# Optimization experiments

Hardware: AMD Instinct MI355X
Metric: run time of the kernel (lower is better)

The kernel has to match this reference:

```python
import jax, jax.numpy as jnp
import numpy as np

B, C, F_IN, F_OUT = 4096, 63, 250, 250
NEG_SLOPE = 0.2  # GATConv default negative_slope


def setup_inputs() -> dict:
    key = jax.random.key(0)
    ks = jax.random.split(key, 5)
    return {
        "x": jax.random.normal(ks[0], (B, 1, C, F_IN), dtype=jnp.float32),
        "W": jax.random.normal(ks[1], (F_IN, F_OUT), dtype=jnp.float32) / np.sqrt(F_IN),
        "att_src": jax.random.normal(ks[2], (F_OUT,), dtype=jnp.float32) / np.sqrt(F_OUT),
        "att_dst": jax.random.normal(ks[3], (F_OUT,), dtype=jnp.float32) / np.sqrt(F_OUT),
        "bias": jax.random.normal(ks[4], (F_OUT,), dtype=jnp.float32) * 0.01,
    }


def reference(x, W, att_src, att_dst, bias):
    # x: [B, 1, C, F_in] -> per-batch graph of C=63 nodes, fully connected
    # (all i!=j edges plus GATConv's default self-loops => dense C x C attention).
    h = jnp.einsum("bcf,fo->bco", x[:, 0], W)          # [B, C, F_out] node embeddings
    a_s = jnp.einsum("bco,o->bc", h, att_src)           # per-source score
    a_d = jnp.einsum("bco,o->bc", h, att_dst)           # per-destination score
    # e[b, dst, src] = leakyrelu(a_s[src] + a_d[dst]); softmax over sources per dst
    e = jax.nn.leaky_relu(a_s[:, None, :] + a_d[:, :, None], NEG_SLOPE)  # [B, C, C]
    alpha = jax.nn.softmax(e, axis=-1)
    out = jnp.einsum("bds,bso->bdo", alpha, h) + bias   # [B, C, F_out]
    return out[:, None]                                  # [B, 1, C, F_out]
```

## Files before the change

### kernel.cpp

```cpp
#include <hip/hip_runtime.h>
#include <hip/hip_bf16.h>

typedef __bf16 bf16;
typedef __attribute__((ext_vector_type(8))) __bf16 bf16x8;
typedef __attribute__((ext_vector_type(4))) __bf16 bf16x4;
typedef __attribute__((ext_vector_type(2))) __bf16 bf16x2;
typedef __attribute__((ext_vector_type(4))) float f32x4;

#define C_NODES 63
#define F_DIM   250
#define NEG_SLOPE 0.2f

#define OFF_AS    32000
#define OFF_AD    32256
#define LDS_BYTES 32768

__device__ __forceinline__ int swz(int a) { return a ^ ((a >> 3) & 0x70); }
__device__ __forceinline__ int swzA(int a) {
    return a ^ ((((a >> 8) & 3) ^ ((a >> 10) & 3)) << 4) ^ (((a >> 12) & 1) << 6);
}

extern "C" __global__ __launch_bounds__(256)
void gat_prep(const float* __restrict__ W, const float* __restrict__ att_src,
              const float* __restrict__ att_dst, bf16* __restrict__ Wp) {
    int i = blockIdx.x * 256 + threadIdx.x;
    int tile = i >> 9;
    int ln   = (i >> 3) & 63;
    int j    = i & 7;
    int kt = tile >> 4, nt = tile & 15;
    int k = kt * 32 + (ln >> 4) * 8 + j;
    int n = nt * 16 + (ln & 15);
    float v = 0.f;
    if (k < F_DIM) {
        if (n < F_DIM) {
            v = W[k * F_DIM + n];
        } else if (n == F_DIM || n == F_DIM + 1) {
            const float* att = (n == F_DIM) ? att_src : att_dst;
            float s = 0.f;
            for (int o = 0; o < F_DIM; ++o) s = fmaf(W[k * F_DIM + o], att[o], s);
            v = s;
        }
    }
    Wp[i] = (bf16)v;
}

extern "C" __global__ __launch_bounds__(256, 4)
void gat_main(const float* __restrict__ x, const bf16* __restrict__ Wp,
              const float* __restrict__ bias, float* __restrict__ out)
{
    __shared__ __align__(16) unsigned char smem[LDS_BYTES];
    const int tid  = threadIdx.x;
    const int lane = tid & 63;
    const int w    = tid >> 6;
    const int b    = blockIdx.x;
    const int fl   = lane & 15;
    const int fh   = lane >> 4;

    const bf16x8* wpv = (const bf16x8*)Wp;

    if (tid < 64) {
        int base = swzA((((tid >> 4) * 8 + 7) << 10) + (48 + (tid & 15)) * 16);
        *(unsigned int*)(smem + base + 4) = 0u;
        *(unsigned long long*)(smem + base + 8) = 0ull;
    } else if (tid < 96) {
        int idx = tid - 64;
        int base = swzA(((24 + (idx >> 2)) << 10) + ((((idx & 3) << 4) | 15) * 16));
        *(f32x4*)(smem + base) = (f32x4){0.f, 0.f, 0.f, 0.f};
    }

    {
        const float* xb = x + (size_t)b * (C_NODES * F_DIM);
#pragma unroll
        for (int it = 0; it < 8; ++it) {
            int idx = tid + it * 256;
            if (idx < 2016) {
                int r = idx >> 5, g = idx & 31;
                const float* src = xb + r * F_DIM + g * 8;
                int dl = (r & 15) | ((g & 3) << 4);
                int base = swzA((((r >> 4) * 8 + (g >> 2)) << 10) + dl * 16);
                if (g < 31) {
                    float2 v0 = *(const float2*)(src);
                    float2 v1 = *(const float2*)(src + 2);
                    float2 v2 = *(const float2*)(src + 4);
                    float2 v3 = *(const float2*)(src + 6);
                    bf16x8 pk = { (bf16)v0.x, (bf16)v0.y, (bf16)v1.x, (bf16)v1.y,
                                  (bf16)v2.x, (bf16)v2.y, (bf16)v3.x, (bf16)v3.y };
                    *(bf16x8*)(smem + base) = pk;
                } else {
                    float2 v0 = *(const float2*)(src);
                    bf16x2 pk = { (bf16)v0.x, (bf16)v0.y };
                    *(bf16x2*)(smem + base) = pk;
                }
            }
        }
    }
    __syncthreads();

    f32x4 acc[4][4];
#pragma unroll
    for (int mt = 0; mt < 4; ++mt)
#pragma unroll
        for (int nti = 0; nti < 4; ++nti)
            acc[mt][nti] = (f32x4){0.f, 0.f, 0.f, 0.f};
#pragma unroll 2
    for (int kt = 0; kt < 8; ++kt) {
        bf16x8 af[4], bw[4];
#pragma unroll
        for (int nti = 0; nti < 4; ++nti)
            bw[nti] = wpv[(kt * 16 + (w * 4 + nti)) * 64 + lane];
#pragma unroll
        for (int mt = 0; mt < 4; ++mt)
            af[mt] = *(const bf16x8*)(smem + swzA(((mt * 8 + kt) << 10) + lane * 16));
#pragma unroll
        for (int mt = 0; mt < 4; ++mt)
#pragma unroll
            for (int nti = 0; nti < 4; ++nti)
                acc[mt][nti] = __builtin_amdgcn_mfma_f32_16x16x32_bf16(
                    af[mt], bw[nti], acc[mt][nti], 0, 0, 0);
    }
    __syncthreads();

    {
#pragma unroll
        for (int mt = 0; mt < 4; ++mt) {
            int s0 = mt * 16 + fh * 4;
#pragma unroll
            for (int nti = 0; nti < 4; ++nti) {
                int f = w * 64 + nti * 16 + fl;
                if (f < F_DIM) {
                    f32x4 v = acc[mt][nti];
                    bf16x4 hv = { (bf16)v.x, (bf16)v.y, (bf16)v.z, (bf16)v.w };
                    *(bf16x4*)(smem + swz(f * 128 + s0 * 2)) = hv;
                }
            }
        }
        if (w == 3 && (fl == 10 || fl == 11)) {
            float* dst = (float*)(smem + (fl == 10 ? OFF_AS : OFF_AD));
#pragma unroll
            for (int mt = 0; mt < 4; ++mt) {
                f32x4 v = acc[mt][3];
#pragma unroll
                for (int i = 0; i < 4; ++i) dst[mt * 16 + fh * 4 + i] = v[i];
            }
        }
    }
    __syncthreads();

    bf16x8 aal[4][2];
    {
        const float* AS  = (const float*)(smem + OFF_AS);
        const float* ADp = (const float*)(smem + OFF_AD);
        f32x4 s0 = *(const f32x4*)(AS + fh * 8);
        f32x4 s1 = *(const f32x4*)(AS + fh * 8 + 4);
        f32x4 s2 = *(const f32x4*)(AS + 32 + fh * 8);
        f32x4 s3 = *(const f32x4*)(AS + 32 + fh * 8 + 4);
#pragma unroll
        for (int mt = 0; mt < 4; ++mt) {
            float ad_v = ADp[mt * 16 + fl];
            float p[16];
#pragma unroll
            for (int k = 0; k < 4; ++k) {
                float e;
                e = s0[k] + ad_v; p[k]      = (e > 0.f) ? e : NEG_SLOPE * e;
                e = s1[k] + ad_v; p[4 + k]  = (e > 0.f) ? e : NEG_SLOPE * e;
                e = s2[k] + ad_v; p[8 + k]  = (e > 0.f) ? e : NEG_SLOPE * e;
                e = s3[k] + ad_v; p[12 + k] = (e > 0.f) ? e : NEG_SLOPE * e;
            }
            if (fh == 3) p[15] = -3.0e38f;
            float md = p[0];
#pragma unroll
            for (int k = 1; k < 16; ++k) md = fmaxf(md, p[k]);
            md = fmaxf(md, __shfl_xor(md, 16));
            md = fmaxf(md, __shfl_xor(md, 32));
            float sum = 0.f;
#pragma unroll
            for (int k = 0; k < 16; ++k) { p[k] = __expf(p[k] - md); sum += p[k]; }
            sum += __shfl_xor(sum, 16);
            sum += __shfl_xor(sum, 32);
            float rz = 1.f / sum;
            bf16x8 a0, a1;
#pragma unroll
            for (int k = 0; k < 8; ++k) {
                a0[k] = (bf16)(p[k] * rz);
                a1[k] = (bf16)(p[8 + k] * rz);
            }
            aal[mt][0] = a0;
            aal[mt][1] = a1;
        }
    }

    f32x4 acc2[4][4];
#pragma unroll
    for (int mt = 0; mt < 4; ++mt)
#pragma unroll
        for (int nti = 0; nti < 4; ++nti)
            acc2[mt][nti] = (f32x4){0.f, 0.f, 0.f, 0.f};
#pragma unroll
    for (int ks = 0; ks < 2; ++ks) {
        int kk = ks * 32 + fh * 8;
        bf16x8 hbf[4];
#pragma unroll
        for (int nti = 0; nti < 4; ++nti) {
            int f = w * 64 + nti * 16 + fl;
            hbf[nti] = *(const bf16x8*)(smem + swz(f * 128 + kk * 2));
        }
#pragma unroll
        for (int mt = 0; mt < 4; ++mt)
#pragma unroll
            for (int nti = 0; nti < 4; ++nti)
                acc2[mt][nti] = __builtin_amdgcn_mfma_f32_16x16x32_bf16(
                    aal[mt][ks], hbf[nti], acc2[mt][nti], 0, 0, 0);
    }

    float bv[4];
#pragma unroll
    for (int nti = 0; nti < 4; ++nti) {
        int f = w * 64 + nti * 16 + fl;
        bv[nti] = (f < F_DIM) ? bias[f] : 0.f;
    }
    float* ob = out + (size_t)b * (C_NODES * F_DIM);
#pragma unroll
    for (int mt = 0; mt < 4; ++mt) {
#pragma unroll
        for (int i = 0; i < 4; ++i) {
            int r = mt * 16 + fh * 4 + i;
            if (r < C_NODES) {
#pragma unroll
                for (int nti = 0; nti < 4; ++nti) {
                    int f = w * 64 + nti * 16 + fl;
                    if (f < F_DIM) ob[r * F_DIM + f] = acc2[mt][nti][i] + bv[nti];
                }
            }
        }
    }
}

extern "C" void kernel_launch(void* const* d_in, const int* in_sizes, int n_in,
                              void* d_out, int out_size, void* d_ws, size_t ws_size,
                              hipStream_t stream) {
    const float* x       = (const float*)d_in[0];
    const float* W       = (const float*)d_in[1];
    const float* att_src = (const float*)d_in[2];
    const float* att_dst = (const float*)d_in[3];
    const float* bias    = (const float*)d_in[4];
    float* out = (float*)d_out;
    bf16* Wp = (bf16*)d_ws;

    gat_prep<<<256, 256, 0, stream>>>(W, att_src, att_dst, Wp);
    gat_main<<<4096, 256, 0, stream>>>(x, Wp, bias, out);
}
```

Measured before the change: 154.6 us.

## Use 512-thread blocks with 8 waves and share softmax alpha through LDS

Doubles the block to 8 waves, so each wave computes 32 output features instead of 64, which halves per-wave accumulator registers. The softmax is now computed once per block (8 threads per destination row), written as bf16 to a new LDS region, and read back as the MFMA A operand. Before, each wave recomputed the full softmax in registers. The aim is higher occupancy and latency hiding for this memory-bound kernel, at the cost of more LDS per block and an extra barrier.

Result: faster. 145.5 us (-5.9%).

```diff
diff --git a/kernel.cpp b/kernel.cpp
--- a/kernel.cpp
+++ b/kernel.cpp
@@ -13,7 +13,8 @@
 
 #define OFF_AS    32000
 #define OFF_AD    32256
-#define LDS_BYTES 32768
+#define OFF_ALPHA 32768
+#define LDS_BYTES 40960
 
 __device__ __forceinline__ int swz(int a) { return a ^ ((a >> 3) & 0x70); }
 __device__ __forceinline__ int swzA(int a) {
@@ -44,7 +45,7 @@
     Wp[i] = (bf16)v;
 }
 
-extern "C" __global__ __launch_bounds__(256, 4)
+extern "C" __global__ __launch_bounds__(512, 8)
 void gat_main(const float* __restrict__ x, const bf16* __restrict__ Wp,
               const float* __restrict__ bias, float* __restrict__ out)
 {
@@ -71,8 +72,8 @@
     {
         const float* xb = x + (size_t)b * (C_NODES * F_DIM);
 #pragma unroll
-        for (int it = 0; it < 8; ++it) {
-            int idx = tid + it * 256;
+        for (int it = 0; it < 4; ++it) {
+            int idx = tid + it * 512;
             if (idx < 2016) {
                 int r = idx >> 5, g = idx & 31;
                 const float* src = xb + r * F_DIM + g * 8;
@@ -96,27 +97,22 @@
     }
     __syncthreads();
 
-    f32x4 acc[4][4];
-#pragma unroll
-    for (int mt = 0; mt < 4; ++mt)
-#pragma unroll
-        for (int nti = 0; nti < 4; ++nti)
-            acc[mt][nti] = (f32x4){0.f, 0.f, 0.f, 0.f};
-#pragma unroll 2
+    f32x4 acc[4][2];
+#pragma unroll
+    for (int mt = 0; mt < 4; ++mt) {
+        acc[mt][0] = (f32x4){0.f, 0.f, 0.f, 0.f};
+        acc[mt][1] = (f32x4){0.f, 0.f, 0.f, 0.f};
+    }
+#pragma unroll 1
     for (int kt = 0; kt < 8; ++kt) {
-        bf16x8 af[4], bw[4];
-#pragma unroll
-        for (int nti = 0; nti < 4; ++nti)
-            bw[nti] = wpv[(kt * 16 + (w * 4 + nti)) * 64 + lane];
-#pragma unroll
-        for (int mt = 0; mt < 4; ++mt)
-            af[mt] = *(const bf16x8*)(smem + swzA(((mt * 8 + kt) << 10) + lane * 16));
-#pragma unroll
-        for (int mt = 0; mt < 4; ++mt)
-#pragma unroll
-            for (int nti = 0; nti < 4; ++nti)
-                acc[mt][nti] = __builtin_amdgcn_mfma_f32_16x16x32_bf16(
-                    af[mt], bw[nti], acc[mt][nti], 0, 0, 0);
+        bf16x8 bw0 = wpv[(kt * 16 + w * 2)     * 64 + lane];
+        bf16x8 bw1 = wpv[(kt * 16 + w * 2 + 1) * 64 + lane];
+#pragma unroll
+        for (int mt = 0; mt < 4; ++mt) {
+            bf16x8 af = *(const bf16x8*)(smem + swzA(((mt * 8 + kt) << 10) + lane * 16));
+            acc[mt][0] = __builtin_amdgcn_mfma_f32_16x16x32_bf16(af, bw0, acc[mt][0], 0, 0, 0);
+            acc[mt][1] = __builtin_amdgcn_mfma_f32_16x16x32_bf16(af, bw1, acc[mt][1], 0, 0, 0);
+        }
     }
     __syncthreads();
 
@@ -125,8 +121,8 @@
         for (int mt = 0; mt < 4; ++mt) {
             int s0 = mt * 16 + fh * 4;
 #pragma unroll
-            for (int nti = 0; nti < 4; ++nti) {
-                int f = w * 64 + nti * 16 + fl;
+            for (int nti = 0; nti < 2; ++nti) {
+                int f = w * 32 + nti * 16 + fl;
                 if (f < F_DIM) {
                     f32x4 v = acc[mt][nti];
                     bf16x4 hv = { (bf16)v.x, (bf16)v.y, (bf16)v.z, (bf16)v.w };
@@ -134,11 +130,11 @@
                 }
             }
         }
-        if (w == 3 && (fl == 10 || fl == 11)) {
+        if (w == 7 && (fl == 10 || fl == 11)) {
             float* dst = (float*)(smem + (fl == 10 ? OFF_AS : OFF_AD));
 #pragma unroll
             for (int mt = 0; mt < 4; ++mt) {
-                f32x4 v = acc[mt][3];
+                f32x4 v = acc[mt][1];
 #pragma unroll
                 for (int i = 0; i < 4; ++i) dst[mt * 16 + fh * 4 + i] = v[i];
             }
@@ -146,76 +142,70 @@
     }
     __syncthreads();
 
-    bf16x8 aal[4][2];
     {
         const float* AS  = (const float*)(smem + OFF_AS);
         const float* ADp = (const float*)(smem + OFF_AD);
-        f32x4 s0 = *(const f32x4*)(AS + fh * 8);
-        f32x4 s1 = *(const f32x4*)(AS + fh * 8 + 4);
-        f32x4 s2 = *(const f32x4*)(AS + 32 + fh * 8);
-        f32x4 s3 = *(const f32x4*)(AS + 32 + fh * 8 + 4);
-#pragma unroll
-        for (int mt = 0; mt < 4; ++mt) {
-            float ad_v = ADp[mt * 16 + fl];
-            float p[16];
-#pragma unroll
-            for (int k = 0; k < 4; ++k) {
-                float e;
-                e = s0[k] + ad_v; p[k]      = (e > 0.f) ? e : NEG_SLOPE * e;
-                e = s1[k] + ad_v; p[4 + k]  = (e > 0.f) ? e : NEG_SLOPE * e;
-                e = s2[k] + ad_v; p[8 + k]  = (e > 0.f) ? e : NEG_SLOPE * e;
-                e = s3[k] + ad_v; p[12 + k] = (e > 0.f) ? e : NEG_SLOPE * e;
-            }
-            if (fh == 3) p[15] = -3.0e38f;
-            float md = p[0];
-#pragma unroll
-            for (int k = 1; k < 16; ++k) md = fmaxf(md, p[k]);
-            md = fmaxf(md, __shfl_xor(md, 16));
-            md = fmaxf(md, __shfl_xor(md, 32));
-            float sum = 0.f;
-#pragma unroll
-            for (int k = 0; k < 16; ++k) { p[k] = __expf(p[k] - md); sum += p[k]; }
-            sum += __shfl_xor(sum, 16);
-            sum += __shfl_xor(sum, 32);
-            float rz = 1.f / sum;
-            bf16x8 a0, a1;
-#pragma unroll
-            for (int k = 0; k < 8; ++k) {
-                a0[k] = (bf16)(p[k] * rz);
-                a1[k] = (bf16)(p[8 + k] * rz);
-            }
-            aal[mt][0] = a0;
-            aal[mt][1] = a1;
-        }
-    }
-
-    f32x4 acc2[4][4];
-#pragma unroll
-    for (int mt = 0; mt < 4; ++mt)
-#pragma unroll
-        for (int nti = 0; nti < 4; ++nti)
-            acc2[mt][nti] = (f32x4){0.f, 0.f, 0.f, 0.f};
-#pragma unroll
+        int d = tid >> 3;
+        int c = tid & 7;
+        float ad_v = ADp[d];
+        f32x4 a0 = *(const f32x4*)(AS + c * 8);
+        f32x4 a1 = *(const f32x4*)(AS + c * 8 + 4);
+        float p[8];
+#pragma unroll
+        for (int k = 0; k < 4; ++k) {
+            float e;
+            e = a0[k] + ad_v; p[k]     = (e > 0.f) ? e : NEG_SLOPE * e;
+            e = a1[k] + ad_v; p[4 + k] = (e > 0.f) ? e : NEG_SLOPE * e;
+        }
+        if (c == 7) p[7] = -3.0e38f;
+        float md = p[0];
+#pragma unroll
+        for (int k = 1; k < 8; ++k) md = fmaxf(md, p[k]);
+        md = fmaxf(md, __shfl_xor(md, 1));
+        md = fmaxf(md, __shfl_xor(md, 2));
+        md = fmaxf(md, __shfl_xor(md, 4));
+        float sum = 0.f;
+#pragma unroll
+        for (int k = 0; k < 8; ++k) { p[k] = __expf(p[k] - md); sum += p[k]; }
+        sum += __shfl_xor(sum, 1);
+        sum += __shfl_xor(sum, 2);
+        sum += __shfl_xor(sum, 4);
+        float rz = 1.f / sum;
+        bf16x8 pk;
+#pragma unroll
+        for (int k = 0; k < 8; ++k) pk[k] = (bf16)(p[k] * rz);
+        *(bf16x8*)(smem + swz(OFF_ALPHA + d * 128 + c * 16)) = pk;
+    }
+    __syncthreads();
+
+    f32x4 acc2[4][2];
+#pragma unroll
+    for (int mt = 0; mt < 4; ++mt) {
+        acc2[mt][0] = (f32x4){0.f, 0.f, 0.f, 0.f};
+        acc2[mt][1] = (f32x4){0.f, 0.f, 0.f, 0.f};
+    }
+#pragma unroll 1
     for (int ks = 0; ks < 2; ++ks) {
         int kk = ks * 32 + fh * 8;
-        bf16x8 hbf[4];
-#pragma unroll
-        for (int nti = 0; nti < 4; ++nti) {
-            int f = w * 64 + nti * 16 + fl;
-            hbf[nti] = *(const bf16x8*)(smem + swz(f * 128 + kk * 2));
-        }
-#pragma unroll
-        for (int mt = 0; mt < 4; ++mt)
-#pragma unroll
-            for (int nti = 0; nti < 4; ++nti)
-                acc2[mt][nti] = __builtin_amdgcn_mfma_f32_16x16x32_bf16(
-                    aal[mt][ks], hbf[nti], acc2[mt][nti], 0, 0, 0);
-    }
-
-    float bv[4];
-#pragma unroll
-    for (int nti = 0; nti < 4; ++nti) {
-        int f = w * 64 + nti * 16 + fl;
+        bf16x8 hbf0, hbf1;
+        {
+            int f0 = w * 32 + fl;
+            int f1 = f0 + 16;
+            hbf0 = *(const bf16x8*)(smem + swz(f0 * 128 + kk * 2));
+            hbf1 = *(const bf16x8*)(smem + swz(f1 * 128 + kk * 2));
+        }
+#pragma unroll
+        for (int mt = 0; mt < 4; ++mt) {
+            bf16x8 aal = *(const bf16x8*)(smem + swz(OFF_ALPHA + (mt * 16 + fl) * 128 + kk * 2));
+            acc2[mt][0] = __builtin_amdgcn_mfma_f32_16x16x32_bf16(aal, hbf0, acc2[mt][0], 0, 0, 0);
+            acc2[mt][1] = __builtin_amdgcn_mfma_f32_16x16x32_bf16(aal, hbf1, acc2[mt][1], 0, 0, 0);
+        }
+    }
+
+    float bv[2];
+#pragma unroll
+    for (int nti = 0; nti < 2; ++nti) {
+        int f = w * 32 + nti * 16 + fl;
         bv[nti] = (f < F_DIM) ? bias[f] : 0.f;
     }
     float* ob = out + (size_t)b * (C_NODES * F_DIM);
@@ -226,8 +216,8 @@
             int r = mt * 16 + fh * 4 + i;
             if (r < C_NODES) {
 #pragma unroll
-                for (int nti = 0; nti < 4; ++nti) {
-                    int f = w * 64 + nti * 16 + fl;
+                for (int nti = 0; nti < 2; ++nti) {
+                    int f = w * 32 + nti * 16 + fl;
                     if (f < F_DIM) ob[r * F_DIM + f] = acc2[mt][nti][i] + bv[nti];
                 }
             }
@@ -247,5 +237,5 @@
     bf16* Wp = (bf16*)d_ws;
 
     gat_prep<<<256, 256, 0, stream>>>(W, att_src, att_dst, Wp);
-    gat_main<<<4096, 256, 0, stream>>>(x, Wp, bias, out);
-}
+    gat_main<<<4096, 512, 0, stream>>>(x, Wp, bias, out);
+}
```
